# Kernel tuning notes

Measured on AMD Instinct MI355X. Metric: run time of the kernel, lower is better.

The kernel has to match this reference:

```python
import jax, jax.numpy as jnp
import numpy as np

ANCHORS = np.array([[10,13],[16,30],[33,23],[30,61],[62,45],[59,119],[116,90],[156,198],[373,326]], dtype=np.float32)
STRIDES = np.array([8,8,8,16,16,16,32,32,32], dtype=np.float32)
MASK = np.array([0,1,2])
NUM_CLASSES = 80
INPUTWIDTH = 416


def _iou(b1, b2):
    # elementwise IoU of xyxy boxes, broadcasting over leading dims
    lt = jnp.maximum(b1[..., :2], b2[..., :2])
    rb = jnp.minimum(b1[..., 2:], b2[..., 2:])
    inter = jnp.clip(rb - lt, 0.0).prod(-1)
    a1 = (b1[..., 2] - b1[..., 0]) * (b1[..., 3] - b1[..., 1])
    a2 = (b2[..., 2] - b2[..., 0]) * (b2[..., 3] - b2[..., 1])
    return inter / (a1 + a2 - inter)


def _bce(p, t):
    # torch BCELoss clamps log at -100
    logp = jnp.maximum(jnp.log(p), -100.0)
    log1p = jnp.maximum(jnp.log(1.0 - p), -100.0)
    return -(t * logp + (1.0 - t) * log1p)


def setup_inputs() -> dict:
    key = jax.random.key(0)
    k1, k2, k3, k4 = jax.random.split(key, 4)
    B, S, NC, G = 32, 52, NUM_CLASSES, 200
    prediction = jax.random.normal(k1, (B, 3 * (5 + NC), S, S), dtype=jnp.float32)
    label = jax.random.randint(k2, (G,), 0, NC).astype(jnp.float32)
    cxy = jax.random.uniform(k3, (G, 2), minval=0.05, maxval=0.95)
    wh = jax.random.uniform(k4, (G, 2), minval=0.02, maxval=0.3)
    bidx = ((jnp.arange(G) * B) // G).astype(jnp.float32)  # sorted, last == B-1
    gt = jnp.concatenate([label[:, None], cxy, wh, bidx[:, None]], axis=1).astype(jnp.float32)
    return {"prediction": prediction, "gt": gt}


def reference(prediction, gt):
    anchors = jnp.asarray(ANCHORS / STRIDES[:, None])  # anchors in grid units
    anch = anchors[jnp.asarray(MASK)]                  # [3,2]
    stride = float(STRIDES[MASK[0]])
    mapsize = 416.0 / stride
    areas = float(INPUTWIDTH ** 2)
    NC = NUM_CLASSES

    B, C, W, H = prediction.shape
    p = prediction.reshape(B, 3, W, H, 5 + NC)
    cxp = jax.nn.sigmoid(p[..., 0])
    cyp = jax.nn.sigmoid(p[..., 1])
    wp = p[..., 2]
    hp = p[..., 3]
    confp = jax.nn.sigmoid(p[..., 4])
    classesp = jax.nn.sigmoid(p[..., 5:])

    grid = jnp.arange(W, dtype=cxp.dtype)
    predx = cxp + grid[None, None, None, :]   # x_coord varies along last axis
    predy = cyp + grid[None, None, :, None]   # y_coord varies along axis -2
    predw = jnp.exp(wp) * anch[:, 0].reshape(1, 3, 1, 1)
    predh = jnp.exp(hp) * anch[:, 1].reshape(1, 3, 1, 1)

    G = gt.shape[0]
    bs = gt[:, 5].astype(jnp.int32)
    label = gt[:, 0].astype(jnp.int32)
    cx = gt[:, 1] * mapsize
    cy = gt[:, 2] * mapsize
    gw = gt[:, 3] * mapsize
    gh = gt[:, 4] * mapsize
    ix = jnp.floor(cx).astype(jnp.int32)
    iy = jnp.floor(cy).astype(jnp.int32)

    gt_xyxy = jnp.stack([cx - gw * 0.5, cy - gh * 0.5, cx + gw * 0.5, cy + gh * 0.5], -1)  # [G,4]
    anch_xyxy = jnp.stack([cx[:, None] - anch[None, :, 0] * 0.5,
                           cy[:, None] - anch[None, :, 1] * 0.5,
                           cx[:, None] + anch[None, :, 0] * 0.5,
                           cy[:, None] + anch[None, :, 1] * 0.5], -1)  # [G,3,4]
    iou_a = _iou(gt_xyxy[:, None, :], anch_xyxy)  # [G,3]
    m = iou_a > 0.3

    Bg = jnp.broadcast_to(bs[:, None], (G, 3))
    Ag = jnp.broadcast_to(jnp.arange(3)[None, :], (G, 3))
    Yg = jnp.broadcast_to(iy[:, None], (G, 3))
    Xi = jnp.broadcast_to(ix[:, None], (G, 3))
    Xm = jnp.where(m, Xi, W)  # OOB index -> dropped by scatter for unmatched anchors

    z = jnp.zeros((B, 3, W, H), prediction.dtype)

    def scat(v):  # scatter [G,3]-broadcastable values into the target grid
        return z.at[Bg, Ag, Xm, Yg].set(jnp.broadcast_to(v, (G, 3)), mode='drop')

    objectness = scat(jnp.ones((G, 3), prediction.dtype))
    offsetctx = scat((cx - jnp.floor(cx))[:, None])
    offsetcty = scat((cy - jnp.floor(cy))[:, None])
    offsetw = scat(jnp.log(gw[:, None] / anch[None, :, 0]))
    offseth = scat(jnp.log(gh[:, None] / anch[None, :, 1]))
    scale_g = 2.0 - (gw * stride) * (gh * stride) / areas  # boxloss_scale per gt
    smallscales = scat(scale_g[:, None])
    Lg = jnp.broadcast_to(label[:, None], (G, 3))
    classes = jnp.zeros((B, 3, W, H, NC), prediction.dtype).at[Bg, Ag, Xm, Yg, Lg].set(1.0, mode='drop')

    # gather decoded predictions at assigned cells (all 3 anchors, mask applied in reductions)
    px = predx[Bg, Ag, Xi, Yg]
    py = predy[Bg, Ag, Xi, Yg]
    pw = predw[Bg, Ag, Xi, Yg]
    ph = predh[Bg, Ag, Xi, Yg]
    pred_xyxy = jnp.stack([px - pw * 0.5, py - ph * 0.5, px + pw * 0.5, py + ph * 0.5], -1)
    pgiou = _iou(gt_xyxy[:, None, :], pred_xyxy)  # [G,3]

    mf = m.astype(prediction.dtype)
    nmask = mf.sum()
    lossiou = jnp.where(nmask > 0,
                        ((1.0 - pgiou) * scale_g[:, None] * mf).sum() / jnp.maximum(nmask, 1.0),
                        jnp.zeros((), prediction.dtype))

    lossx = jnp.mean(smallscales * _bce(cxp, offsetctx))
    lossy = jnp.mean(smallscales * _bce(cyp, offsetcty))
    lossw = jnp.mean((wp * smallscales - offsetw * smallscales) ** 2)
    lossh = jnp.mean((hp * smallscales - offseth * smallscales) ** 2)
    lossobj = jnp.mean(_bce(confp, objectness))
    lossclasses = jnp.mean(_bce(classesp, classes))

    denom = classes.sum() + 1e-10
    recall50 = ((pgiou > 0.5) & m).sum().astype(prediction.dtype) / denom
    recall75 = ((pgiou > 0.75) & m).sum().astype(prediction.dtype) / denom

    loss = lossx + lossy + lossw + lossh + lossobj + lossclasses + lossiou
    return (loss, lossx, lossy, lossw, lossh, lossobj, lossclasses, lossiou, recall50, recall75)
```

## Files before the change

kernel.cpp:

```cpp
#include <hip/hip_runtime.h>

__constant__ float c_aw[3] = {1.25f, 2.0f, 4.125f};
__constant__ float c_ah[3] = {1.625f, 3.75f, 2.875f};

#define LOG2E 1.4426950408889634f
#define LN2   0.6931471805599453f
#define NBLK  2048
#define MAXG  256

__device__ __forceinline__ float softplus_fast(float v) {
    float a = fabsf(v);
    float e = __builtin_amdgcn_exp2f(-a * LOG2E);
    float l = __builtin_amdgcn_logf(1.0f + e) * LN2;
    return fmaxf(v, 0.0f) + l;
}

__device__ __forceinline__ float bce_logit(float v, float t) {
    float l1p = fmaxf(-softplus_fast(v),  -100.0f);
    float lp  = fmaxf(-softplus_fast(-v), -100.0f);
    return -(t * lp + (1.0f - t) * l1p);
}

__device__ __forceinline__ float iou_box(float ax0, float ay0, float ax1, float ay1,
                                         float bx0, float by0, float bx1, float by1) {
    float ltx = fmaxf(ax0, bx0), lty = fmaxf(ay0, by0);
    float rbx = fminf(ax1, bx1), rby = fminf(ay1, by1);
    float iw = fmaxf(rbx - ltx, 0.0f), ih = fmaxf(rby - lty, 0.0f);
    float inter = iw * ih;
    float a1 = (ax1 - ax0) * (ay1 - ay0);
    float a2 = (bx1 - bx0) * (by1 - by0);
    return inter / (a1 + a2 - inter);
}


__global__ void __launch_bounds__(256) yolo_main(const float4* __restrict__ p4, int n4,
                                                 const float* __restrict__ pred,
                                                 const float* __restrict__ gt, int G,
                                                 float* __restrict__ cls_part,
                                                 float* __restrict__ obj_part,
                                                 float* __restrict__ sp_part, int sblk) {
    int tid = threadIdx.x;
    int lane = tid & 63;
    int wave = tid >> 6;

    float atot = 0.0f, askip = 0.0f, aobj = 0.0f;
    const float C100 = 100.0f * LOG2E;
    int i = blockIdx.x * 256 + tid;
    int r = (i * 4) % 85;
    for (; i < n4; i += NBLK * 256) {
        float4 v = p4[i];
        float vs[4] = {v.x, v.y, v.z, v.w};
        float s[4];
#pragma unroll
        for (int j = 0; j < 4; ++j) {
            float t = __builtin_amdgcn_exp2f(vs[j] * LOG2E);
            s[j] = fminf(__builtin_amdgcn_logf(1.0f + t), C100);
            atot += s[j];
        }
        askip += (r < 5) ? s[0] : 0.0f;
        askip += (r < 4 || r >= 84) ? s[1] : 0.0f;
        askip += (r < 3 || r >= 83) ? s[2] : 0.0f;
        askip += (r < 2 || r >= 82) ? s[3] : 0.0f;
        aobj  += (r == 4) ? s[0] : 0.0f;
        aobj  += (r == 3) ? s[1] : 0.0f;
        aobj  += (r == 2) ? s[2] : 0.0f;
        aobj  += (r == 1) ? s[3] : 0.0f;
        r += 32;
        r = (r >= 85) ? r - 85 : r;
    }
    float acls = (atot - askip) * LN2;
    float aob  = aobj * LN2;
#pragma unroll
    for (int off = 32; off > 0; off >>= 1) {
        acls += __shfl_down(acls, off);
        aob  += __shfl_down(aob, off);
    }
    __shared__ float rc[4], ro[4];
    if (lane == 0) { rc[wave] = acls; ro[wave] = aob; }
    __syncthreads();
    if (tid == 0) {
        cls_part[blockIdx.x] = rc[0] + rc[1] + rc[2] + rc[3];
        obj_part[blockIdx.x] = ro[0] + ro[1] + ro[2] + ro[3];
    }

    if (blockIdx.x < (unsigned)sblk) {
        __shared__ float s_cx[MAXG], s_cy[MAXG], s_gw[MAXG], s_gh[MAXG], s_sc[MAXG];
        __shared__ int s_ix[MAXG], s_iy[MAXG], s_bs[MAXG], s_lab[MAXG];
        __shared__ unsigned char s_m[3 * MAXG];
        __shared__ float acc[11];
        if (tid < 11) acc[tid] = 0.0f;

        for (int g = tid; g < G; g += blockDim.x) {
            float lab = gt[g * 6 + 0];
            float cx  = gt[g * 6 + 1] * 52.0f;
            float cy  = gt[g * 6 + 2] * 52.0f;
            float gw  = gt[g * 6 + 3] * 52.0f;
            float gh  = gt[g * 6 + 4] * 52.0f;
            float bn  = gt[g * 6 + 5];
            s_cx[g] = cx; s_cy[g] = cy; s_gw[g] = gw; s_gh[g] = gh;
            s_ix[g] = (int)floorf(cx); s_iy[g] = (int)floorf(cy);
            s_bs[g] = (int)bn; s_lab[g] = (int)lab;
            s_sc[g] = 2.0f - (gw * 8.0f) * (gh * 8.0f) / 173056.0f;
        }
        __syncthreads();

        for (int t = tid; t < 3 * G; t += blockDim.x) {
            int g = t / 3, a = t % 3;
            float cx = s_cx[g], cy = s_cy[g], gw = s_gw[g], gh = s_gh[g];
            float aw = c_aw[a], ah = c_ah[a];
            float iou = iou_box(cx - gw * 0.5f, cy - gh * 0.5f,
                                cx + gw * 0.5f, cy + gh * 0.5f,
                                cx - aw * 0.5f, cy - ah * 0.5f,
                                cx + aw * 0.5f, cy + ah * 0.5f);
            s_m[t] = (iou > 0.3f) ? 1 : 0;
        }
        __syncthreads();

        int t = blockIdx.x * 4 + wave;
        bool active = (t < 3 * G) && s_m[t];
        if (active) {
            int g = t / 3, a = t % 3;
            int ix = s_ix[g], iy = s_iy[g], bs = s_bs[g], lab = s_lab[g];
            bool ohit = false, rhit = false;
            for (int g2 = g + 1 + lane; g2 < G; g2 += 64) {
                if (s_m[g2 * 3 + a] && s_bs[g2] == bs && s_ix[g2] == ix && s_iy[g2] == iy) {
                    ohit = true;
                    if (s_lab[g2] == lab) rhit = true;
                }
            }
            bool owner = !__any(ohit);
            bool rep   = !__any(rhit);

            if (lane == 0) {
                float cx = s_cx[g], cy = s_cy[g], gw = s_gw[g], gh = s_gh[g], sc = s_sc[g];
                float aw = c_aw[a], ah = c_ah[a];
                int base = ((bs * 3 + a) * 2704 + ix * 52 + iy) * 85;
                float v0 = pred[base + 0], v1 = pred[base + 1], v2 = pred[base + 2];
                float v3 = pred[base + 3], v4 = pred[base + 4];
                float px = 1.0f / (1.0f + __builtin_amdgcn_exp2f(-v0 * LOG2E)) + (float)iy;
                float py = 1.0f / (1.0f + __builtin_amdgcn_exp2f(-v1 * LOG2E)) + (float)ix;
                float pw = __builtin_amdgcn_exp2f(v2 * LOG2E) * aw;
                float ph = __builtin_amdgcn_exp2f(v3 * LOG2E) * ah;
                float pg = iou_box(cx - gw * 0.5f, cy - gh * 0.5f,
                                   cx + gw * 0.5f, cy + gh * 0.5f,
                                   px - pw * 0.5f, py - ph * 0.5f,
                                   px + pw * 0.5f, py + ph * 0.5f);
                atomicAdd(&acc[7], 1.0f);
                atomicAdd(&acc[6], (1.0f - pg) * sc);
                if (pg > 0.5f)  atomicAdd(&acc[8], 1.0f);
                if (pg > 0.75f) atomicAdd(&acc[9], 1.0f);
                if (owner) {
                    float tx = cx - floorf(cx);
                    float ty = cy - floorf(cy);
                    float ow = __builtin_amdgcn_logf(gw / aw) * LN2;
                    float oh = __builtin_amdgcn_logf(gh / ah) * LN2;
                    atomicAdd(&acc[0], sc * bce_logit(v0, tx));
                    atomicAdd(&acc[1], sc * bce_logit(v1, ty));
                    float dw = v2 * sc - ow * sc;
                    float dh = v3 * sc - oh * sc;
                    atomicAdd(&acc[2], dw * dw);
                    atomicAdd(&acc[3], dh * dh);
                    atomicAdd(&acc[4], bce_logit(v4, 1.0f) - bce_logit(v4, 0.0f));
                }
                if (rep) {
                    float vc = pred[base + 5 + lab];
                    atomicAdd(&acc[5], bce_logit(vc, 1.0f) - bce_logit(vc, 0.0f));
                    atomicAdd(&acc[10], 1.0f);
                }
            }
        }
        __syncthreads();
        if (tid < 11) sp_part[blockIdx.x * 11 + tid] = acc[tid];
    }
}

__global__ void __launch_bounds__(256) finalize_k(const float* __restrict__ cls_part,
                                                  const float* __restrict__ obj_part,
                                                  const float* __restrict__ sp_part, int sblk,
                                                  float* __restrict__ out) {
    float c = 0.0f, o = 0.0f;
    for (int i = threadIdx.x; i < NBLK; i += 256) {
        c += cls_part[i];
        o += obj_part[i];
    }
    float a[11];
#pragma unroll
    for (int k = 0; k < 11; ++k) a[k] = 0.0f;
    for (int b = threadIdx.x; b < sblk; b += 256) {
#pragma unroll
        for (int k = 0; k < 11; ++k) a[k] += sp_part[b * 11 + k];
    }
#pragma unroll
    for (int off = 32; off > 0; off >>= 1) {
        c += __shfl_down(c, off);
        o += __shfl_down(o, off);
#pragma unroll
        for (int k = 0; k < 11; ++k) a[k] += __shfl_down(a[k], off);
    }
    __shared__ float red[4][13];
    int wave = threadIdx.x >> 6, lane = threadIdx.x & 63;
    if (lane == 0) {
        red[wave][0] = c; red[wave][1] = o;
#pragma unroll
        for (int k = 0; k < 11; ++k) red[wave][2 + k] = a[k];
    }
    __syncthreads();
    if (threadIdx.x == 0) {
        float s[13];
#pragma unroll
        for (int k = 0; k < 13; ++k)
            s[k] = red[0][k] + red[1][k] + red[2][k] + red[3][k];
        float cls_base = s[0], obj_base = s[1];
        float SX = s[2], SY = s[3], SW = s[4], SH = s[5], OBJC = s[6], CLSC = s[7];
        float IOUS = s[8], NMASK = s[9], R50 = s[10], R75 = s[11], DEN = s[12];
        const float NCELL = 259584.0f;
        const float NCLSE = 20766720.0f;
        float lossx = SX / NCELL;
        float lossy = SY / NCELL;
        float lossw = SW / NCELL;
        float lossh = SH / NCELL;
        float lossobj = (obj_base + OBJC) / NCELL;
        float losscls = (cls_base + CLSC) / NCLSE;
        float lossiou = (NMASK > 0.0f) ? (IOUS / fmaxf(NMASK, 1.0f)) : 0.0f;
        float denom = DEN + 1e-10f;
        float r50 = R50 / denom;
        float r75 = R75 / denom;
        float loss = lossx + lossy + lossw + lossh + lossobj + losscls + lossiou;
        out[0] = loss;  out[1] = lossx;   out[2] = lossy;   out[3] = lossw; out[4] = lossh;
        out[5] = lossobj; out[6] = losscls; out[7] = lossiou; out[8] = r50; out[9] = r75;
    }
}

extern "C" void kernel_launch(void* const* d_in, const int* in_sizes, int n_in,
                              void* d_out, int out_size, void* d_ws, size_t ws_size,
                              hipStream_t stream) {
    const float* pred = (const float*)d_in[0];
    const float* gtp  = (const float*)d_in[1];
    float* out = (float*)d_out;
    float* ws  = (float*)d_ws;
    int ntot = in_sizes[0];
    int G    = in_sizes[1] / 6;

    float* cls_part = ws;
    float* obj_part = ws + NBLK;
    float* sp_part  = ws + 2 * NBLK;
    int sblk = (3 * G + 3) / 4;

    int n4 = ntot / 4;
    yolo_main<<<NBLK, 256, 0, stream>>>((const float4*)pred, n4, pred, gtp, G,
                                        cls_part, obj_part, sp_part, sblk);
    finalize_k<<<1, 256, 0, stream>>>(cls_part, obj_part, sp_part, sblk, out);
}
```

Before: 26.30 us.

## Split blocks into dedicated sparse-GT blocks and streaming blocks with nontemporal loads

Before, every block first streamed the dense prediction tensor and then, for the first sblk blocks, also ran the per-GT matching work. Now the first 150 blocks do only the sparse GT/anchor work and the remaining blocks do only the dense softplus reduction. That keeps the dense stream off the critical path of the GT blocks, so they no longer sit at the tail. The dense loads become nontemporal, and the residue step changes to 27 to match the new grid stride. SPBLK is hardcoded to 150, which assumes 3*G/4 equals 150 (G=200), so other G values would be handled wrongly.

After: 24.20 us. 8.0% less time.

```diff
diff --git a/kernel.cpp b/kernel.cpp
--- a/kernel.cpp
+++ b/kernel.cpp
@@ -6,7 +6,11 @@
 #define LOG2E 1.4426950408889634f
 #define LN2   0.6931471805599453f
 #define NBLK  2048
+#define SPBLK 150
+#define NDB   (NBLK - SPBLK)
 #define MAXG  256
+
+typedef float floatx4 __attribute__((ext_vector_type(4)));
 
 __device__ __forceinline__ float softplus_fast(float v) {
     float a = fabsf(v);
@@ -33,160 +37,163 @@
 }
 
 
-__global__ void __launch_bounds__(256) yolo_main(const float4* __restrict__ p4, int n4,
+__global__ void __launch_bounds__(256) yolo_main(const floatx4* __restrict__ p4, int n4,
                                                  const float* __restrict__ pred,
                                                  const float* __restrict__ gt, int G,
                                                  float* __restrict__ cls_part,
                                                  float* __restrict__ obj_part,
-                                                 float* __restrict__ sp_part, int sblk) {
+                                                 float* __restrict__ sp_part) {
     int tid = threadIdx.x;
     int lane = tid & 63;
     int wave = tid >> 6;
 
-    float atot = 0.0f, askip = 0.0f, aobj = 0.0f;
-    const float C100 = 100.0f * LOG2E;
-    int i = blockIdx.x * 256 + tid;
-    int r = (i * 4) % 85;
-    for (; i < n4; i += NBLK * 256) {
-        float4 v = p4[i];
-        float vs[4] = {v.x, v.y, v.z, v.w};
-        float s[4];
-#pragma unroll
-        for (int j = 0; j < 4; ++j) {
-            float t = __builtin_amdgcn_exp2f(vs[j] * LOG2E);
-            s[j] = fminf(__builtin_amdgcn_logf(1.0f + t), C100);
-            atot += s[j];
-        }
-        askip += (r < 5) ? s[0] : 0.0f;
-        askip += (r < 4 || r >= 84) ? s[1] : 0.0f;
-        askip += (r < 3 || r >= 83) ? s[2] : 0.0f;
-        askip += (r < 2 || r >= 82) ? s[3] : 0.0f;
-        aobj  += (r == 4) ? s[0] : 0.0f;
-        aobj  += (r == 3) ? s[1] : 0.0f;
-        aobj  += (r == 2) ? s[2] : 0.0f;
-        aobj  += (r == 1) ? s[3] : 0.0f;
-        r += 32;
-        r = (r >= 85) ? r - 85 : r;
-    }
-    float acls = (atot - askip) * LN2;
-    float aob  = aobj * LN2;
-#pragma unroll
-    for (int off = 32; off > 0; off >>= 1) {
-        acls += __shfl_down(acls, off);
-        aob  += __shfl_down(aob, off);
-    }
-    __shared__ float rc[4], ro[4];
-    if (lane == 0) { rc[wave] = acls; ro[wave] = aob; }
-    __syncthreads();
-    if (tid == 0) {
-        cls_part[blockIdx.x] = rc[0] + rc[1] + rc[2] + rc[3];
-        obj_part[blockIdx.x] = ro[0] + ro[1] + ro[2] + ro[3];
-    }
-
-    if (blockIdx.x < (unsigned)sblk) {
-        __shared__ float s_cx[MAXG], s_cy[MAXG], s_gw[MAXG], s_gh[MAXG], s_sc[MAXG];
-        __shared__ int s_ix[MAXG], s_iy[MAXG], s_bs[MAXG], s_lab[MAXG];
-        __shared__ unsigned char s_m[3 * MAXG];
-        __shared__ float acc[11];
-        if (tid < 11) acc[tid] = 0.0f;
-
-        for (int g = tid; g < G; g += blockDim.x) {
-            float lab = gt[g * 6 + 0];
-            float cx  = gt[g * 6 + 1] * 52.0f;
-            float cy  = gt[g * 6 + 2] * 52.0f;
-            float gw  = gt[g * 6 + 3] * 52.0f;
-            float gh  = gt[g * 6 + 4] * 52.0f;
-            float bn  = gt[g * 6 + 5];
-            s_cx[g] = cx; s_cy[g] = cy; s_gw[g] = gw; s_gh[g] = gh;
-            s_ix[g] = (int)floorf(cx); s_iy[g] = (int)floorf(cy);
-            s_bs[g] = (int)bn; s_lab[g] = (int)lab;
-            s_sc[g] = 2.0f - (gw * 8.0f) * (gh * 8.0f) / 173056.0f;
-        }
+    if (blockIdx.x >= SPBLK) {
+        int bd = blockIdx.x - SPBLK;
+        float atot = 0.0f, askip = 0.0f, aobj = 0.0f;
+        const float C100 = 100.0f * LOG2E;
+        int i = bd * 256 + tid;
+        int r = (i * 4) % 85;
+        const int stride = NDB * 256;
+        for (; i < n4; i += stride) {
+            floatx4 v = __builtin_nontemporal_load(&p4[i]);
+            float vs[4] = {v.x, v.y, v.z, v.w};
+            float s[4];
+#pragma unroll
+            for (int j = 0; j < 4; ++j) {
+                float t = __builtin_amdgcn_exp2f(vs[j] * LOG2E);
+                s[j] = fminf(__builtin_amdgcn_logf(1.0f + t), C100);
+                atot += s[j];
+            }
+            askip += (r < 5) ? s[0] : 0.0f;
+            askip += (r < 4 || r >= 84) ? s[1] : 0.0f;
+            askip += (r < 3 || r >= 83) ? s[2] : 0.0f;
+            askip += (r < 2 || r >= 82) ? s[3] : 0.0f;
+            aobj  += (r == 4) ? s[0] : 0.0f;
+            aobj  += (r == 3) ? s[1] : 0.0f;
+            aobj  += (r == 2) ? s[2] : 0.0f;
+            aobj  += (r == 1) ? s[3] : 0.0f;
+            r += 27;
+            r = (r >= 85) ? r - 85 : r;
+        }
+        float acls = (atot - askip) * LN2;
+        float aob  = aobj * LN2;
+#pragma unroll
+        for (int off = 32; off > 0; off >>= 1) {
+            acls += __shfl_down(acls, off);
+            aob  += __shfl_down(aob, off);
+        }
+        __shared__ float rc[4], ro[4];
+        if (lane == 0) { rc[wave] = acls; ro[wave] = aob; }
         __syncthreads();
-
-        for (int t = tid; t < 3 * G; t += blockDim.x) {
-            int g = t / 3, a = t % 3;
-            float cx = s_cx[g], cy = s_cy[g], gw = s_gw[g], gh = s_gh[g];
+        if (tid == 0) {
+            cls_part[bd] = rc[0] + rc[1] + rc[2] + rc[3];
+            obj_part[bd] = ro[0] + ro[1] + ro[2] + ro[3];
+        }
+        return;
+    }
+
+    __shared__ float s_cx[MAXG], s_cy[MAXG], s_gw[MAXG], s_gh[MAXG], s_sc[MAXG];
+    __shared__ int s_ix[MAXG], s_iy[MAXG], s_bs[MAXG], s_lab[MAXG];
+    __shared__ unsigned char s_m[3 * MAXG];
+    __shared__ float acc[11];
+    if (tid < 11) acc[tid] = 0.0f;
+
+    for (int g = tid; g < G; g += blockDim.x) {
+        float lab = gt[g * 6 + 0];
+        float cx  = gt[g * 6 + 1] * 52.0f;
+        float cy  = gt[g * 6 + 2] * 52.0f;
+        float gw  = gt[g * 6 + 3] * 52.0f;
+        float gh  = gt[g * 6 + 4] * 52.0f;
+        float bn  = gt[g * 6 + 5];
+        s_cx[g] = cx; s_cy[g] = cy; s_gw[g] = gw; s_gh[g] = gh;
+        s_ix[g] = (int)floorf(cx); s_iy[g] = (int)floorf(cy);
+        s_bs[g] = (int)bn; s_lab[g] = (int)lab;
+        s_sc[g] = 2.0f - (gw * 8.0f) * (gh * 8.0f) / 173056.0f;
+    }
+    __syncthreads();
+
+    for (int t = tid; t < 3 * G; t += blockDim.x) {
+        int g = t / 3, a = t % 3;
+        float cx = s_cx[g], cy = s_cy[g], gw = s_gw[g], gh = s_gh[g];
+        float aw = c_aw[a], ah = c_ah[a];
+        float iou = iou_box(cx - gw * 0.5f, cy - gh * 0.5f,
+                            cx + gw * 0.5f, cy + gh * 0.5f,
+                            cx - aw * 0.5f, cy - ah * 0.5f,
+                            cx + aw * 0.5f, cy + ah * 0.5f);
+        s_m[t] = (iou > 0.3f) ? 1 : 0;
+    }
+    __syncthreads();
+
+    int t = blockIdx.x * 4 + wave;
+    bool active = (t < 3 * G) && s_m[t];
+    if (active) {
+        int g = t / 3, a = t % 3;
+        int ix = s_ix[g], iy = s_iy[g], bs = s_bs[g], lab = s_lab[g];
+        bool ohit = false, rhit = false;
+        for (int g2 = g + 1 + lane; g2 < G; g2 += 64) {
+            if (s_m[g2 * 3 + a] && s_bs[g2] == bs && s_ix[g2] == ix && s_iy[g2] == iy) {
+                ohit = true;
+                if (s_lab[g2] == lab) rhit = true;
+            }
+        }
+        bool owner = !__any(ohit);
+        bool rep   = !__any(rhit);
+
+        if (lane == 0) {
+            float cx = s_cx[g], cy = s_cy[g], gw = s_gw[g], gh = s_gh[g], sc = s_sc[g];
             float aw = c_aw[a], ah = c_ah[a];
-            float iou = iou_box(cx - gw * 0.5f, cy - gh * 0.5f,
-                                cx + gw * 0.5f, cy + gh * 0.5f,
-                                cx - aw * 0.5f, cy - ah * 0.5f,
-                                cx + aw * 0.5f, cy + ah * 0.5f);
-            s_m[t] = (iou > 0.3f) ? 1 : 0;
-        }
-        __syncthreads();
-
-        int t = blockIdx.x * 4 + wave;
-        bool active = (t < 3 * G) && s_m[t];
-        if (active) {
-            int g = t / 3, a = t % 3;
-            int ix = s_ix[g], iy = s_iy[g], bs = s_bs[g], lab = s_lab[g];
-            bool ohit = false, rhit = false;
-            for (int g2 = g + 1 + lane; g2 < G; g2 += 64) {
-                if (s_m[g2 * 3 + a] && s_bs[g2] == bs && s_ix[g2] == ix && s_iy[g2] == iy) {
-                    ohit = true;
-                    if (s_lab[g2] == lab) rhit = true;
-                }
-            }
-            bool owner = !__any(ohit);
-            bool rep   = !__any(rhit);
-
-            if (lane == 0) {
-                float cx = s_cx[g], cy = s_cy[g], gw = s_gw[g], gh = s_gh[g], sc = s_sc[g];
-                float aw = c_aw[a], ah = c_ah[a];
-                int base = ((bs * 3 + a) * 2704 + ix * 52 + iy) * 85;
-                float v0 = pred[base + 0], v1 = pred[base + 1], v2 = pred[base + 2];
-                float v3 = pred[base + 3], v4 = pred[base + 4];
-                float px = 1.0f / (1.0f + __builtin_amdgcn_exp2f(-v0 * LOG2E)) + (float)iy;
-                float py = 1.0f / (1.0f + __builtin_amdgcn_exp2f(-v1 * LOG2E)) + (float)ix;
-                float pw = __builtin_amdgcn_exp2f(v2 * LOG2E) * aw;
-                float ph = __builtin_amdgcn_exp2f(v3 * LOG2E) * ah;
-                float pg = iou_box(cx - gw * 0.5f, cy - gh * 0.5f,
-                                   cx + gw * 0.5f, cy + gh * 0.5f,
-                                   px - pw * 0.5f, py - ph * 0.5f,
-                                   px + pw * 0.5f, py + ph * 0.5f);
-                atomicAdd(&acc[7], 1.0f);
-                atomicAdd(&acc[6], (1.0f - pg) * sc);
-                if (pg > 0.5f)  atomicAdd(&acc[8], 1.0f);
-                if (pg > 0.75f) atomicAdd(&acc[9], 1.0f);
-                if (owner) {
-                    float tx = cx - floorf(cx);
-                    float ty = cy - floorf(cy);
-                    float ow = __builtin_amdgcn_logf(gw / aw) * LN2;
-                    float oh = __builtin_amdgcn_logf(gh / ah) * LN2;
-                    atomicAdd(&acc[0], sc * bce_logit(v0, tx));
-                    atomicAdd(&acc[1], sc * bce_logit(v1, ty));
-                    float dw = v2 * sc - ow * sc;
-                    float dh = v3 * sc - oh * sc;
-                    atomicAdd(&acc[2], dw * dw);
-                    atomicAdd(&acc[3], dh * dh);
-                    atomicAdd(&acc[4], bce_logit(v4, 1.0f) - bce_logit(v4, 0.0f));
-                }
-                if (rep) {
-                    float vc = pred[base + 5 + lab];
-                    atomicAdd(&acc[5], bce_logit(vc, 1.0f) - bce_logit(vc, 0.0f));
-                    atomicAdd(&acc[10], 1.0f);
-                }
-            }
-        }
-        __syncthreads();
-        if (tid < 11) sp_part[blockIdx.x * 11 + tid] = acc[tid];
-    }
+            int base = ((bs * 3 + a) * 2704 + ix * 52 + iy) * 85;
+            float v0 = pred[base + 0], v1 = pred[base + 1], v2 = pred[base + 2];
+            float v3 = pred[base + 3], v4 = pred[base + 4];
+            float px = 1.0f / (1.0f + __builtin_amdgcn_exp2f(-v0 * LOG2E)) + (float)iy;
+            float py = 1.0f / (1.0f + __builtin_amdgcn_exp2f(-v1 * LOG2E)) + (float)ix;
+            float pw = __builtin_amdgcn_exp2f(v2 * LOG2E) * aw;
+            float ph = __builtin_amdgcn_exp2f(v3 * LOG2E) * ah;
+            float pg = iou_box(cx - gw * 0.5f, cy - gh * 0.5f,
+                               cx + gw * 0.5f, cy + gh * 0.5f,
+                               px - pw * 0.5f, py - ph * 0.5f,
+                               px + pw * 0.5f, py + ph * 0.5f);
+            atomicAdd(&acc[7], 1.0f);
+            atomicAdd(&acc[6], (1.0f - pg) * sc);
+            if (pg > 0.5f)  atomicAdd(&acc[8], 1.0f);
+            if (pg > 0.75f) atomicAdd(&acc[9], 1.0f);
+            if (owner) {
+                float tx = cx - floorf(cx);
+                float ty = cy - floorf(cy);
+                float ow = __builtin_amdgcn_logf(gw / aw) * LN2;
+                float oh = __builtin_amdgcn_logf(gh / ah) * LN2;
+                atomicAdd(&acc[0], sc * bce_logit(v0, tx));
+                atomicAdd(&acc[1], sc * bce_logit(v1, ty));
+                float dw = v2 * sc - ow * sc;
+                float dh = v3 * sc - oh * sc;
+                atomicAdd(&acc[2], dw * dw);
+                atomicAdd(&acc[3], dh * dh);
+                atomicAdd(&acc[4], bce_logit(v4, 1.0f) - bce_logit(v4, 0.0f));
+            }
+            if (rep) {
+                float vc = pred[base + 5 + lab];
+                atomicAdd(&acc[5], bce_logit(vc, 1.0f) - bce_logit(vc, 0.0f));
+                atomicAdd(&acc[10], 1.0f);
+            }
+        }
+    }
+    __syncthreads();
+    if (tid < 11) sp_part[blockIdx.x * 11 + tid] = acc[tid];
 }
 
 __global__ void __launch_bounds__(256) finalize_k(const float* __restrict__ cls_part,
                                                   const float* __restrict__ obj_part,
-                                                  const float* __restrict__ sp_part, int sblk,
+                                                  const float* __restrict__ sp_part,
                                                   float* __restrict__ out) {
     float c = 0.0f, o = 0.0f;
-    for (int i = threadIdx.x; i < NBLK; i += 256) {
+    for (int i = threadIdx.x; i < NDB; i += 256) {
         c += cls_part[i];
         o += obj_part[i];
     }
     float a[11];
 #pragma unroll
     for (int k = 0; k < 11; ++k) a[k] = 0.0f;
-    for (int b = threadIdx.x; b < sblk; b += 256) {
+    for (int b = threadIdx.x; b < SPBLK; b += 256) {
 #pragma unroll
         for (int k = 0; k < 11; ++k) a[k] += sp_part[b * 11 + k];
     }
@@ -242,12 +249,11 @@
     int G    = in_sizes[1] / 6;
 
     float* cls_part = ws;
-    float* obj_part = ws + NBLK;
-    float* sp_part  = ws + 2 * NBLK;
-    int sblk = (3 * G + 3) / 4;
+    float* obj_part = ws + NDB;
+    float* sp_part  = ws + 2 * NDB;
 
     int n4 = ntot / 4;
-    yolo_main<<<NBLK, 256, 0, stream>>>((const float4*)pred, n4, pred, gtp, G,
-                                        cls_part, obj_part, sp_part, sblk);
-    finalize_k<<<1, 256, 0, stream>>>(cls_part, obj_part, sp_part, sblk, out);
-}
+    yolo_main<<<NBLK, 256, 0, stream>>>((const floatx4*)pred, n4, pred, gtp, G,
+                                        cls_part, obj_part, sp_part);
+    finalize_k<<<1, 256, 0, stream>>>(cls_part, obj_part, sp_part, out);
+}
```
